# Kernel tuning notes

Measured on AMD Instinct MI355X. Metric: run time of the kernel, lower is better.

Reference implementation:

```python
import jax, jax.numpy as jnp
import numpy as np
import math

EPS = 1e-5
NUM_HEADS = 16


def _ln(x, g, b):
    m = jnp.mean(x, axis=-1, keepdims=True)
    v = jnp.mean(jnp.square(x - m), axis=-1, keepdims=True)
    return (x - m) * jax.lax.rsqrt(v + EPS) * g + b


def setup_inputs() -> dict:
    key = jax.random.key(0)
    ks = jax.random.split(key, 20)
    B, S, D = 16, 256, 1024
    G, L, QL = 576, 64, 16
    V = L * QL
    s = 0.02
    inp = {
        "hidden_states": jax.random.normal(ks[0], (B, S, D), jnp.float32),
        "global_ctx": jax.random.normal(ks[1], (B, G, D), jnp.float32),
        "vision_pos": jax.random.randint(ks[2], (B, G), 0, 1000),
        "instruct_pos": jax.random.randint(ks[3], (B, L), 0, 1000),
        "queries": jax.random.normal(ks[4], (B, V, D), jnp.float32),
        "image_tokens": jax.random.normal(ks[5], (B, V, D), jnp.float32),
        "query_len": QL,
        "W_in": jax.random.normal(ks[6], (D, 2 * D), jnp.float32) * s,
        "W_ctx": jax.random.normal(ks[7], (D, D), jnp.float32) * s,
        "ln_q_g": jnp.ones((D,), jnp.float32),
        "ln_q_b": jnp.zeros((D,), jnp.float32),
        "Wq": jax.random.normal(ks[8], (D, D), jnp.float32) * s,
        "ln_k_g": jnp.ones((D,), jnp.float32),
        "ln_k_b": jnp.zeros((D,), jnp.float32),
        "Wk": jax.random.normal(ks[9], (D, D), jnp.float32) * s,
        "ln_v_g": jnp.ones((D,), jnp.float32),
        "ln_v_b": jnp.zeros((D,), jnp.float32),
        "Wv": jax.random.normal(ks[10], (D, D), jnp.float32) * s,
        "Wo": jax.random.normal(ks[11], (D, D), jnp.float32) * s,
        "norm_g": jnp.ones((D,), jnp.float32),
        "norm_b": jnp.zeros((D,), jnp.float32),
        "W1": jax.random.normal(ks[12], (D, D), jnp.float32) * s,
        "W2": jax.random.normal(ks[13], (D, D), jnp.float32) * s,
    }
    return inp


def reference(hidden_states, global_ctx, vision_pos, instruct_pos, queries,
              image_tokens, query_len, W_in, W_ctx, ln_q_g, ln_q_b, Wq,
              ln_k_g, ln_k_b, Wk, ln_v_g, ln_v_b, Wv, Wo, norm_g, norm_b,
              W1, W2):
    B, V, _ = queries.shape
    D = hidden_states.shape[-1]
    G = global_ctx.shape[1]
    L = instruct_pos.shape[1]
    H = NUM_HEADS
    hd = D // H
    scale = 1.0 / math.sqrt(hd)
    Hq = int(math.sqrt(query_len))          # query grid side
    Hgc = int(math.sqrt(G))                 # ctx grid side
    Hw = Hgc // Hq                          # window side
    Wt = Hw * Hw                            # tokens per window

    residual = image_tokens
    # proj_in on concatenated queries
    pq = jnp.concatenate([queries, image_tokens], axis=-1) @ W_in.T  # (B,V,D)

    # window extraction: (B,Hgc,Wgc,D) -> (B, query_len, Wt, D)
    win = global_ctx.reshape(B, Hq, Hw, Hq, Hw, D)
    win = win.transpose(0, 1, 3, 2, 4, 5).reshape(B, query_len, Wt, D)
    win = win @ W_ctx.T                      # proj_context, shared across L

    # cross-attention: each query v attends only to window (v mod query_len)
    q = _ln(pq, ln_q_g, ln_q_b) @ Wq.T
    q = q.reshape(B, L, query_len, H, hd)
    k = (_ln(win, ln_k_g, ln_k_b) @ Wk.T).reshape(B, query_len, Wt, H, hd)
    v = (_ln(win, ln_v_g, ln_v_b) @ Wv.T).reshape(B, query_len, Wt, H, hd)

    scores = jnp.einsum('blqhd,bqwhd->blqhw', q, k) * scale
    attn = jax.nn.softmax(scores, axis=-1)
    ao = jnp.einsum('blqhw,bqwhd->blqhd', attn, v).reshape(B, V, D)
    ao = ao @ Wo.T

    x = _ln(ao + pq, norm_g, norm_b)
    out = jax.nn.gelu(x @ W1.T, approximate=False) @ W2.T
    return out + residual
```

## Files before the change

### kernel.cpp

```cpp
#include <hip/hip_runtime.h>
#include <cstdint>
#include <cstddef>

typedef unsigned short u16;
typedef __bf16 bf16_t;
typedef bf16_t bf16x8 __attribute__((ext_vector_type(8)));
typedef float f32x4 __attribute__((ext_vector_type(4)));

#define DEV __device__ __forceinline__
#define AS1 __attribute__((address_space(1)))
#define AS3 __attribute__((address_space(3)))

DEV u16 f2bf(float f) {
  unsigned u = __float_as_uint(f);
  u += 0x7fffu + ((u >> 16) & 1u);
  return (u16)(u >> 16);
}
DEV float bf2f(u16 h) {
  return __uint_as_float(((unsigned)h) << 16);
}

struct Cvt9 {
  const float* s[9];
  u16* d[9];
  long cumv[10];
};

__global__ __launch_bounds__(256)
void convert_batch(Cvt9 jobs) {
  const long total = jobs.cumv[9];
  for (long i = (long)blockIdx.x * 256 + threadIdx.x; i < total;
       i += (long)gridDim.x * 256) {
    int j = 0;
#pragma unroll
    for (int t = 0; t < 8; ++t)
      if (i >= jobs.cumv[t + 1]) j = t + 1;
    const long e = (i - jobs.cumv[j]) * 4;
    float4 v = *(const float4*)(jobs.s[j] + e);
    ushort4 o;
    o.x = f2bf(v.x); o.y = f2bf(v.y); o.z = f2bf(v.z); o.w = f2bf(v.w);
    *(ushort4*)(jobs.d[j] + e) = o;
  }
}

__global__ __launch_bounds__(256)
void build_acat(const float* __restrict__ q, const float* __restrict__ it,
                u16* __restrict__ dst) {
  const long total = 16384l * 2048 / 4;
  for (long i = (long)blockIdx.x * 256 + threadIdx.x; i < total;
       i += (long)gridDim.x * 256) {
    long e = i * 4;
    int m = (int)(e >> 11);
    int k = (int)(e & 2047);
    const float* s = (k < 1024) ? (q + (long)m * 1024 + k)
                                : (it + (long)m * 1024 + (k - 1024));
    float4 v = *(const float4*)s;
    ushort4 o;
    o.x = f2bf(v.x); o.y = f2bf(v.y); o.z = f2bf(v.z); o.w = f2bf(v.w);
    *(ushort4*)(dst + e) = o;
  }
}

__global__ __launch_bounds__(256)
void ln_rows(const float* __restrict__ x, const float* __restrict__ g,
             const float* __restrict__ b, u16* __restrict__ out) {
  __shared__ float red[8];
  const int row = blockIdx.x, tid = threadIdx.x;
  const float* xr = x + (size_t)row * 1024;
  float4 v = *(const float4*)(xr + tid * 4);
  float s = v.x + v.y + v.z + v.w;
  float ss = v.x * v.x + v.y * v.y + v.z * v.z + v.w * v.w;
#pragma unroll
  for (int o = 32; o > 0; o >>= 1) { s += __shfl_xor(s, o); ss += __shfl_xor(ss, o); }
  if ((tid & 63) == 0) { red[tid >> 6] = s; red[4 + (tid >> 6)] = ss; }
  __syncthreads();
  s = red[0] + red[1] + red[2] + red[3];
  ss = red[4] + red[5] + red[6] + red[7];
  const float mean = s * 0.0009765625f;
  const float var = ss * 0.0009765625f - mean * mean;
  const float rinv = rsqrtf(var + 1e-5f);
  const int c = tid * 4;
  float4 gg = *(const float4*)(g + c);
  float4 bb = *(const float4*)(b + c);
  ushort4 o4;
  o4.x = f2bf((v.x - mean) * rinv * gg.x + bb.x);
  o4.y = f2bf((v.y - mean) * rinv * gg.y + bb.y);
  o4.z = f2bf((v.z - mean) * rinv * gg.z + bb.z);
  o4.w = f2bf((v.w - mean) * rinv * gg.w + bb.w);
  *(ushort4*)(out + (size_t)row * 1024 + c) = o4;
}

__global__ __launch_bounds__(256)
void ln_kv(const float* __restrict__ winp,
           const float* __restrict__ gk, const float* __restrict__ bk,
           const float* __restrict__ gv, const float* __restrict__ bv,
           u16* __restrict__ kout, u16* __restrict__ vout) {
  __shared__ float red[8];
  const int m = blockIdx.x, tid = threadIdx.x;
  const int b = m / 576, rem = m % 576;
  const int qw = rem / 36, w = rem % 36;
  const int gidx = (qw >> 2) * 144 + (w / 6) * 24 + (qw & 3) * 6 + (w % 6);
  const float* xr = winp + ((size_t)b * 576 + gidx) * 1024;
  float4 v = *(const float4*)(xr + tid * 4);
  float s = v.x + v.y + v.z + v.w;
  float ss = v.x * v.x + v.y * v.y + v.z * v.z + v.w * v.w;
#pragma unroll
  for (int o = 32; o > 0; o >>= 1) { s += __shfl_xor(s, o); ss += __shfl_xor(ss, o); }
  if ((tid & 63) == 0) { red[tid >> 6] = s; red[4 + (tid >> 6)] = ss; }
  __syncthreads();
  s = red[0] + red[1] + red[2] + red[3];
  ss = red[4] + red[5] + red[6] + red[7];
  const float mean = s * 0.0009765625f;
  const float var = ss * 0.0009765625f - mean * mean;
  const float rinv = rsqrtf(var + 1e-5f);
  const int c = tid * 4;
  float4 gg = *(const float4*)(gk + c);
  float4 bb = *(const float4*)(bk + c);
  float4 g2 = *(const float4*)(gv + c);
  float4 b2 = *(const float4*)(bv + c);
  float nx = (v.x - mean) * rinv, ny = (v.y - mean) * rinv;
  float nz = (v.z - mean) * rinv, nw = (v.w - mean) * rinv;
  ushort4 ok, ov;
  ok.x = f2bf(nx * gg.x + bb.x); ok.y = f2bf(ny * gg.y + bb.y);
  ok.z = f2bf(nz * gg.z + bb.z); ok.w = f2bf(nw * gg.w + bb.w);
  ov.x = f2bf(nx * g2.x + b2.x); ov.y = f2bf(ny * g2.y + b2.y);
  ov.z = f2bf(nz * g2.z + b2.z); ov.w = f2bf(nw * g2.w + b2.w);
  *(ushort4*)(kout + (size_t)m * 1024 + c) = ok;
  *(ushort4*)(vout + (size_t)m * 1024 + c) = ov;
}

template <int EPI>
__global__ __launch_bounds__(512, 2)
void gemm256(const u16* __restrict__ A, const u16* __restrict__ Bw,
             u16* __restrict__ outB, float* __restrict__ outF,
             const float* __restrict__ addF, int M, int N, int K) {
  __shared__ __align__(16) u16 lds[2][2][16384];
  const int tid = threadIdx.x;
  const int wave = tid >> 6, lane = tid & 63;
  const int fr = lane & 15, fq = lane >> 4;
  const int swz = (blockIdx.x & 7) * ((int)gridDim.x >> 3) + (blockIdx.x >> 3);
  const int brow = (swz >> 2) << 8;
  const int bcol = (swz & 3) << 8;

  const int srow = tid >> 3;
  const int cgo = ((tid & 7) ^ (srow & 7)) << 3;
  const u16* pa0 = A + (size_t)(brow + srow) * K + cgo;
  const u16* pb0 = Bw + (size_t)(bcol + srow) * K + cgo;
  const size_t rstep = (size_t)64 * K;

  f32x4 acc[8][4];
#pragma unroll
  for (int mf = 0; mf < 8; ++mf)
#pragma unroll
    for (int nf = 0; nf < 4; ++nf) acc[mf][nf] = (f32x4){0.f, 0.f, 0.f, 0.f};

  const int fx = fr & 7;
  const int arow = (wave >> 2) * 128 + fr;
  const int brl = (wave & 3) * 64 + fr;
  const int ck0 = (fq ^ fx) << 3;
  const int ck1 = ((4 + fq) ^ fx) << 3;

  auto STAGE_A = [&](int buf, int kt) {
    const int k0 = kt << 6;
#pragma unroll
    for (int i = 0; i < 4; ++i)
      __builtin_amdgcn_global_load_lds((const AS1 void*)(pa0 + i * rstep + k0),
                                       (AS3 void*)&lds[buf][0][i * 4096 + tid * 8],
                                       16, 0, 0);
  };
  auto STAGE_B = [&](int buf, int kt) {
    const int k0 = kt << 6;
#pragma unroll
    for (int i = 0; i < 4; ++i)
      __builtin_amdgcn_global_load_lds((const AS1 void*)(pb0 + i * rstep + k0),
                                       (AS3 void*)&lds[buf][1][i * 4096 + tid * 8],
                                       16, 0, 0);
  };

  const int NT = K >> 6;
  STAGE_A(0, 0);
  STAGE_B(0, 0);
  __syncthreads();

  bf16x8 a0[4], a1[4], b0[4], b1[4];
  for (int t = 0; t < NT; ++t) {
    const u16* la = &lds[t & 1][0][0];
    const u16* lb = &lds[t & 1][1][0];
    const int nxt = (t + 1) & 1;

#pragma unroll
    for (int nf = 0; nf < 4; ++nf)
      b0[nf] = *(const bf16x8*)&lb[(brl + nf * 16) * 64 + ck0];
#pragma unroll
    for (int mf = 0; mf < 4; ++mf)
      a0[mf] = *(const bf16x8*)&la[(arow + mf * 16) * 64 + ck0];
#pragma unroll
    for (int mf = 0; mf < 4; ++mf)
      a1[mf] = *(const bf16x8*)&la[(arow + 64 + mf * 16) * 64 + ck0];
    if (t + 1 < NT) STAGE_A(nxt, t + 1);
    __builtin_amdgcn_sched_barrier(0);
    __builtin_amdgcn_s_setprio(1);
#pragma unroll
    for (int mf = 0; mf < 4; ++mf)
#pragma unroll
      for (int nf = 0; nf < 4; ++nf)
        acc[mf][nf] = __builtin_amdgcn_mfma_f32_16x16x32_bf16(a0[mf], b0[nf],
                                                              acc[mf][nf], 0, 0, 0);
    __builtin_amdgcn_s_setprio(0);
#pragma unroll
    for (int nf = 0; nf < 4; ++nf)
      b1[nf] = *(const bf16x8*)&lb[(brl + nf * 16) * 64 + ck1];
#pragma unroll
    for (int mf = 0; mf < 4; ++mf)
      a0[mf] = *(const bf16x8*)&la[(arow + mf * 16) * 64 + ck1];
    __builtin_amdgcn_sched_barrier(0);
    __builtin_amdgcn_s_setprio(1);
#pragma unroll
    for (int mf = 0; mf < 4; ++mf)
#pragma unroll
      for (int nf = 0; nf < 4; ++nf)
        acc[4 + mf][nf] = __builtin_amdgcn_mfma_f32_16x16x32_bf16(a1[mf], b0[nf],
                                                                  acc[4 + mf][nf], 0, 0, 0);
    __builtin_amdgcn_s_setprio(0);
#pragma unroll
    for (int mf = 0; mf < 4; ++mf)
      a1[mf] = *(const bf16x8*)&la[(arow + 64 + mf * 16) * 64 + ck1];
    if (t + 1 < NT) STAGE_B(nxt, t + 1);
    __builtin_amdgcn_sched_barrier(0);
    __builtin_amdgcn_s_setprio(1);
#pragma unroll
    for (int mf = 0; mf < 4; ++mf)
#pragma unroll
      for (int nf = 0; nf < 4; ++nf)
        acc[mf][nf] = __builtin_amdgcn_mfma_f32_16x16x32_bf16(a0[mf], b1[nf],
                                                              acc[mf][nf], 0, 0, 0);
    __builtin_amdgcn_s_setprio(0);
    __builtin_amdgcn_sched_barrier(0);
    __builtin_amdgcn_s_setprio(1);
#pragma unroll
    for (int mf = 0; mf < 4; ++mf)
#pragma unroll
      for (int nf = 0; nf < 4; ++nf)
        acc[4 + mf][nf] = __builtin_amdgcn_mfma_f32_16x16x32_bf16(a1[mf], b1[nf],
                                                                  acc[4 + mf][nf], 0, 0, 0);
    __builtin_amdgcn_s_setprio(0);
    __syncthreads();
  }

#pragma unroll
  for (int mf = 0; mf < 8; ++mf) {
    const int row0 = brow + (wave >> 2) * 128 + mf * 16 + fq * 4;
#pragma unroll
    for (int nf = 0; nf < 4; ++nf) {
      const int col = bcol + (wave & 3) * 64 + nf * 16 + fr;
#pragma unroll
      for (int j = 0; j < 4; ++j) {
        const size_t o = (size_t)(row0 + j) * N + col;
        const float vv = acc[mf][nf][j];
        if constexpr (EPI == 0) {
          outB[o] = f2bf(vv);
        } else if constexpr (EPI == 1) {
          outF[o] = vv;
        } else if constexpr (EPI == 2) {
          outF[o] = vv + addF[o];
        } else {
          outB[o] = f2bf(0.5f * vv * (1.0f + erff(vv * 0.70710678118654752f)));
        }
      }
    }
  }
}

__global__ __launch_bounds__(256)
void attn_kernel(const u16* __restrict__ q, const u16* __restrict__ k,
                 const u16* __restrict__ v, u16* __restrict__ ao) {
  __shared__ __align__(16) u16 Qs[64 * 64];
  __shared__ __align__(16) u16 Ks[36 * 64];
  __shared__ __align__(16) u16 Vs[36 * 64];
  __shared__ float Ps[64 * 36];
  const int bid = blockIdx.x;
  const int h = bid & 15, qw = (bid >> 4) & 15, b = bid >> 8;
  const int tid = threadIdx.x;
  const size_t qbase = ((size_t)b * 1024) * 1024 + (size_t)h * 64;
  for (int i = tid; i < 64 * 16; i += 256) {
    int l = i >> 4, d4 = (i & 15) * 4;
    *(ushort4*)&Qs[l * 64 + d4] =
        *(const ushort4*)&q[qbase + (size_t)(l * 16 + qw) * 1024 + d4];
  }
  const size_t kvbase = ((size_t)(b * 16 + qw)) * 36 * 1024 + (size_t)h * 64;
  for (int i = tid; i < 36 * 16; i += 256) {
    int w = i >> 4, d4 = (i & 15) * 4;
    *(ushort4*)&Ks[w * 64 + d4] = *(const ushort4*)&k[kvbase + (size_t)w * 1024 + d4];
    *(ushort4*)&Vs[w * 64 + d4] = *(const ushort4*)&v[kvbase + (size_t)w * 1024 + d4];
  }
  __syncthreads();
  const int l = tid >> 2, quad = tid & 3;
  float sc[9];
#pragma unroll
  for (int wi = 0; wi < 9; ++wi) {
    int w = quad * 9 + wi;
    float acc = 0.f;
#pragma unroll
    for (int dd = 0; dd < 64; dd += 4) {
      ushort4 qv = *(const ushort4*)&Qs[l * 64 + dd];
      ushort4 kv = *(const ushort4*)&Ks[w * 64 + dd];
      acc += bf2f(qv.x) * bf2f(kv.x) + bf2f(qv.y) * bf2f(kv.y) +
             bf2f(qv.z) * bf2f(kv.z) + bf2f(qv.w) * bf2f(kv.w);
    }
    sc[wi] = acc * 0.125f;
  }
  float mx = sc[0];
#pragma unroll
  for (int wi = 1; wi < 9; ++wi) mx = fmaxf(mx, sc[wi]);
  mx = fmaxf(mx, __shfl_xor(mx, 1));
  mx = fmaxf(mx, __shfl_xor(mx, 2));
  float sum = 0.f;
#pragma unroll
  for (int wi = 0; wi < 9; ++wi) { sc[wi] = __expf(sc[wi] - mx); sum += sc[wi]; }
  sum += __shfl_xor(sum, 1);
  sum += __shfl_xor(sum, 2);
  const float inv = 1.0f / sum;
#pragma unroll
  for (int wi = 0; wi < 9; ++wi) Ps[l * 36 + quad * 9 + wi] = sc[wi] * inv;
  __syncthreads();
  float o[16];
#pragma unroll
  for (int dd = 0; dd < 16; ++dd) o[dd] = 0.f;
  for (int w = 0; w < 36; ++w) {
    float p = Ps[l * 36 + w];
#pragma unroll
    for (int dd = 0; dd < 16; dd += 4) {
      ushort4 vv = *(const ushort4*)&Vs[w * 64 + quad * 16 + dd];
      o[dd] += p * bf2f(vv.x); o[dd + 1] += p * bf2f(vv.y);
      o[dd + 2] += p * bf2f(vv.z); o[dd + 3] += p * bf2f(vv.w);
    }
  }
  const size_t obase = qbase + (size_t)(l * 16 + qw) * 1024 + quad * 16;
#pragma unroll
  for (int dd = 0; dd < 16; dd += 4) {
    ushort4 ov;
    ov.x = f2bf(o[dd]); ov.y = f2bf(o[dd + 1]);
    ov.z = f2bf(o[dd + 2]); ov.w = f2bf(o[dd + 3]);
    *(ushort4*)&ao[obase + dd] = ov;
  }
}

extern "C" void kernel_launch(void* const* d_in, const int* in_sizes, int n_in,
                              void* d_out, int out_size, void* d_ws, size_t ws_size,
                              hipStream_t stream) {
  const float* gctx = (const float*)d_in[1];
  const float* queries = (const float*)d_in[4];
  const float* image_tokens = (const float*)d_in[5];
  const float* W_in = (const float*)d_in[7];
  const float* W_ctx = (const float*)d_in[8];
  const float* ln_q_g = (const float*)d_in[9];
  const float* ln_q_b = (const float*)d_in[10];
  const float* Wq = (const float*)d_in[11];
  const float* ln_k_g = (const float*)d_in[12];
  const float* ln_k_b = (const float*)d_in[13];
  const float* Wk = (const float*)d_in[14];
  const float* ln_v_g = (const float*)d_in[15];
  const float* ln_v_b = (const float*)d_in[16];
  const float* Wv = (const float*)d_in[17];
  const float* Wo = (const float*)d_in[18];
  const float* norm_g = (const float*)d_in[19];
  const float* norm_b = (const float*)d_in[20];
  const float* W1 = (const float*)d_in[21];
  const float* W2 = (const float*)d_in[22];
  float* out = (float*)d_out;

  char* ws = (char*)d_ws;
  const size_t MB = 1024 * 1024;
  u16* w_in_b  = (u16*)(ws + 0 * MB);
  u16* w_ctx_b = (u16*)(ws + 4 * MB);
  u16* wq_b    = (u16*)(ws + 6 * MB);
  u16* wk_b    = (u16*)(ws + 8 * MB);
  u16* wv_b    = (u16*)(ws + 10 * MB);
  u16* wo_b    = (u16*)(ws + 12 * MB);
  u16* w1_b    = (u16*)(ws + 14 * MB);
  u16* w2_b    = (u16*)(ws + 16 * MB);
  char* regA = ws + 18 * MB;
  char* regB = regA + 64 * MB;
  char* regC = regB + 36 * MB;

  u16* acat = (u16*)regA;
  u16* pqln = (u16*)regA;
  u16* qmat = (u16*)(regA + 32 * MB);
  u16* vln  = (u16*)regA;
  u16* aoh  = (u16*)regA;
  u16* xmat = (u16*)(regA + 32 * MB);

  float* winp = (float*)regB;
  u16* kmat = (u16*)regB;
  u16* vmat = (u16*)(regB + 18 * MB);
  u16* gout = (u16*)regB;

  u16* gcb = (u16*)regC;
  u16* kln = (u16*)regC;

  float* pq = out;

  Cvt9 jobs;
  const float* srcs[9] = {W_in, W_ctx, Wq, Wk, Wv, Wo, W1, W2, gctx};
  u16* dsts[9] = {w_in_b, w_ctx_b, wq_b, wk_b, wv_b, wo_b, w1_b, w2_b, gcb};
  long sizes[9] = {2048l * 1024, 1048576, 1048576, 1048576, 1048576,
                   1048576, 1048576, 1048576, 9216l * 1024};
  long cum = 0;
  for (int j = 0; j < 9; ++j) {
    jobs.s[j] = srcs[j];
    jobs.d[j] = dsts[j];
    jobs.cumv[j] = cum;
    cum += sizes[j] / 4;
  }
  jobs.cumv[9] = cum;
  convert_batch<<<dim3(2048), dim3(256), 0, stream>>>(jobs);
  build_acat<<<dim3(8192), dim3(256), 0, stream>>>(queries, image_tokens, acat);

  gemm256<1><<<dim3(256), dim3(512), 0, stream>>>(acat, w_in_b, nullptr, pq,
                                                  nullptr, 16384, 1024, 2048);
  ln_rows<<<dim3(16384), dim3(256), 0, stream>>>(pq, ln_q_g, ln_q_b, pqln);
  gemm256<0><<<dim3(256), dim3(512), 0, stream>>>(pqln, wq_b, qmat, nullptr,
                                                  nullptr, 16384, 1024, 1024);
  gemm256<1><<<dim3(144), dim3(512), 0, stream>>>(gcb, w_ctx_b, nullptr, winp,
                                                  nullptr, 9216, 1024, 1024);
  ln_kv<<<dim3(9216), dim3(256), 0, stream>>>(winp, ln_k_g, ln_k_b, ln_v_g,
                                              ln_v_b, kln, vln);
  gemm256<0><<<dim3(144), dim3(512), 0, stream>>>(kln, wk_b, kmat, nullptr,
                                                  nullptr, 9216, 1024, 1024);
  gemm256<0><<<dim3(144), dim3(512), 0, stream>>>(vln, wv_b, vmat, nullptr,
                                                  nullptr, 9216, 1024, 1024);
  attn_kernel<<<dim3(4096), dim3(256), 0, stream>>>(qmat, kmat, vmat, aoh);
  gemm256<2><<<dim3(256), dim3(512), 0, stream>>>(aoh, wo_b, nullptr, pq, pq,
                                                  16384, 1024, 1024);
  ln_rows<<<dim3(16384), dim3(256), 0, stream>>>(pq, norm_g, norm_b, xmat);
  gemm256<3><<<dim3(256), dim3(512), 0, stream>>>(xmat, w1_b, gout, nullptr,
                                                  nullptr, 16384, 1024, 1024);
  gemm256<2><<<dim3(256), dim3(512), 0, stream>>>(gout, w2_b, nullptr, out,
                                                  image_tokens, 16384, 1024, 1024);
}
```

Before: 522.0 us.

## Use MFMA for window attention with transposed V written by GEMM epilogue

Replaces the scalar FP32 dot-product attention with bf16 MFMA 16x16x32 for both QK^T and PV, using padded LDS tiles. Softmax probabilities are stored as bf16 in LDS. The V projection GEMM gets a new epilogue that writes V transposed per window so PV can load contiguous operands. The aim is to cut the scalar ALU and LDS cost of the attention kernel. In exchange it adds zero-padding work, rounds P to bf16, and makes the V GEMM store scattered.

```diff
diff --git a/kernel.cpp b/kernel.cpp
--- a/kernel.cpp
+++ b/kernel.cpp
@@ -263,8 +263,13 @@
           outF[o] = vv;
         } else if constexpr (EPI == 2) {
           outF[o] = vv + addF[o];
+        } else if constexpr (EPI == 3) {
+          outB[o] = f2bf(0.5f * vv * (1.0f + erff(vv * 0.70710678118654752f)));
         } else {
-          outB[o] = f2bf(0.5f * vv * (1.0f + erff(vv * 0.70710678118654752f)));
+          const int gr = row0 + j;
+          const int bqw = gr / 36;
+          const int wl = gr - bqw * 36;
+          outB[(size_t)bqw * 36864 + (size_t)col * 36 + wl] = f2bf(vv);
         }
       }
     }
@@ -273,75 +278,109 @@
 
 __global__ __launch_bounds__(256)
 void attn_kernel(const u16* __restrict__ q, const u16* __restrict__ k,
-                 const u16* __restrict__ v, u16* __restrict__ ao) {
-  __shared__ __align__(16) u16 Qs[64 * 64];
-  __shared__ __align__(16) u16 Ks[36 * 64];
-  __shared__ __align__(16) u16 Vs[36 * 64];
-  __shared__ float Ps[64 * 36];
+                 const u16* __restrict__ vt, u16* __restrict__ ao) {
+  __shared__ __align__(16) u16 Q_lds[64 * 72];
+  __shared__ __align__(16) u16 K_lds[48 * 72];
+  __shared__ __align__(16) u16 Vt_lds[64 * 72];
+  __shared__ __align__(16) u16 P_lds[64 * 72];
   const int bid = blockIdx.x;
   const int h = bid & 15, qw = (bid >> 4) & 15, b = bid >> 8;
   const int tid = threadIdx.x;
-  const size_t qbase = ((size_t)b * 1024) * 1024 + (size_t)h * 64;
+  const int wave = tid >> 6, lane = tid & 63;
+  const int lq = lane & 15, lk = lane >> 4;
+
+  const size_t qbase = (size_t)b * 1048576 + (size_t)h * 64;
   for (int i = tid; i < 64 * 16; i += 256) {
-    int l = i >> 4, d4 = (i & 15) * 4;
-    *(ushort4*)&Qs[l * 64 + d4] =
-        *(const ushort4*)&q[qbase + (size_t)(l * 16 + qw) * 1024 + d4];
-  }
-  const size_t kvbase = ((size_t)(b * 16 + qw)) * 36 * 1024 + (size_t)h * 64;
+    const int l = i >> 4, c4 = (i & 15) * 4;
+    *(ushort4*)&Q_lds[l * 72 + c4] =
+        *(const ushort4*)&q[qbase + (size_t)(l * 16 + qw) * 1024 + c4];
+  }
+  const size_t kvbase = (size_t)((b * 16 + qw) * 36) * 1024 + (size_t)h * 64;
   for (int i = tid; i < 36 * 16; i += 256) {
-    int w = i >> 4, d4 = (i & 15) * 4;
-    *(ushort4*)&Ks[w * 64 + d4] = *(const ushort4*)&k[kvbase + (size_t)w * 1024 + d4];
-    *(ushort4*)&Vs[w * 64 + d4] = *(const ushort4*)&v[kvbase + (size_t)w * 1024 + d4];
+    const int w = i >> 4, c4 = (i & 15) * 4;
+    *(ushort4*)&K_lds[w * 72 + c4] = *(const ushort4*)&k[kvbase + (size_t)w * 1024 + c4];
+  }
+  const size_t vbase = (size_t)(b * 16 + qw) * 36864 + (size_t)h * 2304;
+  for (int i = tid; i < 64 * 9; i += 256) {
+    const int d = i / 9, w4 = (i - d * 9) * 4;
+    *(ushort4*)&Vt_lds[d * 72 + w4] = *(const ushort4*)&vt[vbase + d * 36 + w4];
+  }
+  const ushort4 z4 = {0, 0, 0, 0};
+  for (int i = tid; i < 64 * 7; i += 256) {
+    const int d = i / 7, w = 36 + (i - d * 7) * 4;
+    *(ushort4*)&Vt_lds[d * 72 + w] = z4;
+  }
+  for (int i = tid; i < 64 * 4; i += 256) {
+    const int m = i >> 2, w = 48 + (i & 3) * 4;
+    *(ushort4*)&P_lds[m * 72 + w] = z4;
   }
   __syncthreads();
-  const int l = tid >> 2, quad = tid & 3;
-  float sc[9];
-#pragma unroll
-  for (int wi = 0; wi < 9; ++wi) {
-    int w = quad * 9 + wi;
-    float acc = 0.f;
-#pragma unroll
-    for (int dd = 0; dd < 64; dd += 4) {
-      ushort4 qv = *(const ushort4*)&Qs[l * 64 + dd];
-      ushort4 kv = *(const ushort4*)&Ks[w * 64 + dd];
-      acc += bf2f(qv.x) * bf2f(kv.x) + bf2f(qv.y) * bf2f(kv.y) +
-             bf2f(qv.z) * bf2f(kv.z) + bf2f(qv.w) * bf2f(kv.w);
+
+  bf16x8 qa[2];
+#pragma unroll
+  for (int ks = 0; ks < 2; ++ks)
+    qa[ks] = *(const bf16x8*)&Q_lds[(wave * 16 + lq) * 72 + ks * 32 + lk * 8];
+  f32x4 accs[3];
+#pragma unroll
+  for (int nt = 0; nt < 3; ++nt) accs[nt] = (f32x4){0.f, 0.f, 0.f, 0.f};
+#pragma unroll
+  for (int nt = 0; nt < 3; ++nt)
+#pragma unroll
+    for (int ks = 0; ks < 2; ++ks) {
+      bf16x8 kb = *(const bf16x8*)&K_lds[(nt * 16 + lq) * 72 + ks * 32 + lk * 8];
+      accs[nt] = __builtin_amdgcn_mfma_f32_16x16x32_bf16(qa[ks], kb, accs[nt], 0, 0, 0);
     }
-    sc[wi] = acc * 0.125f;
-  }
-  float mx = sc[0];
-#pragma unroll
-  for (int wi = 1; wi < 9; ++wi) mx = fmaxf(mx, sc[wi]);
-  mx = fmaxf(mx, __shfl_xor(mx, 1));
-  mx = fmaxf(mx, __shfl_xor(mx, 2));
-  float sum = 0.f;
-#pragma unroll
-  for (int wi = 0; wi < 9; ++wi) { sc[wi] = __expf(sc[wi] - mx); sum += sc[wi]; }
-  sum += __shfl_xor(sum, 1);
-  sum += __shfl_xor(sum, 2);
-  const float inv = 1.0f / sum;
-#pragma unroll
-  for (int wi = 0; wi < 9; ++wi) Ps[l * 36 + quad * 9 + wi] = sc[wi] * inv;
+
+  const bool v2ok = (lq < 4);
+#pragma unroll
+  for (int j = 0; j < 4; ++j) {
+    const float s0 = accs[0][j] * 0.125f;
+    const float s1 = accs[1][j] * 0.125f;
+    const float s2 = v2ok ? accs[2][j] * 0.125f : -1e30f;
+    float mx = fmaxf(fmaxf(s0, s1), s2);
+    mx = fmaxf(mx, __shfl_xor(mx, 1));
+    mx = fmaxf(mx, __shfl_xor(mx, 2));
+    mx = fmaxf(mx, __shfl_xor(mx, 4));
+    mx = fmaxf(mx, __shfl_xor(mx, 8));
+    const float e0 = __expf(s0 - mx);
+    const float e1 = __expf(s1 - mx);
+    const float e2 = v2ok ? __expf(s2 - mx) : 0.f;
+    float sm = e0 + e1 + e2;
+    sm += __shfl_xor(sm, 1);
+    sm += __shfl_xor(sm, 2);
+    sm += __shfl_xor(sm, 4);
+    sm += __shfl_xor(sm, 8);
+    const float inv = 1.0f / sm;
+    const int mrow = wave * 16 + lk * 4 + j;
+    P_lds[mrow * 72 + lq] = f2bf(e0 * inv);
+    P_lds[mrow * 72 + 16 + lq] = f2bf(e1 * inv);
+    P_lds[mrow * 72 + 32 + lq] = f2bf(e2 * inv);
+  }
   __syncthreads();
-  float o[16];
-#pragma unroll
-  for (int dd = 0; dd < 16; ++dd) o[dd] = 0.f;
-  for (int w = 0; w < 36; ++w) {
-    float p = Ps[l * 36 + w];
-#pragma unroll
-    for (int dd = 0; dd < 16; dd += 4) {
-      ushort4 vv = *(const ushort4*)&Vs[w * 64 + quad * 16 + dd];
-      o[dd] += p * bf2f(vv.x); o[dd + 1] += p * bf2f(vv.y);
-      o[dd + 2] += p * bf2f(vv.z); o[dd + 3] += p * bf2f(vv.w);
+
+  bf16x8 va[2];
+#pragma unroll
+  for (int ks = 0; ks < 2; ++ks)
+    va[ks] = *(const bf16x8*)&Vt_lds[(wave * 16 + lq) * 72 + ks * 32 + lk * 8];
+  f32x4 acco[4];
+#pragma unroll
+  for (int nt = 0; nt < 4; ++nt) acco[nt] = (f32x4){0.f, 0.f, 0.f, 0.f};
+#pragma unroll
+  for (int nt = 0; nt < 4; ++nt)
+#pragma unroll
+    for (int ks = 0; ks < 2; ++ks) {
+      bf16x8 pb = *(const bf16x8*)&P_lds[(nt * 16 + lq) * 72 + ks * 32 + lk * 8];
+      acco[nt] = __builtin_amdgcn_mfma_f32_16x16x32_bf16(va[ks], pb, acco[nt], 0, 0, 0);
     }
-  }
-  const size_t obase = qbase + (size_t)(l * 16 + qw) * 1024 + quad * 16;
-#pragma unroll
-  for (int dd = 0; dd < 16; dd += 4) {
+
+#pragma unroll
+  for (int nt = 0; nt < 4; ++nt) {
+    const int m = nt * 16 + lq;
+    const int d0 = wave * 16 + lk * 4;
     ushort4 ov;
-    ov.x = f2bf(o[dd]); ov.y = f2bf(o[dd + 1]);
-    ov.z = f2bf(o[dd + 2]); ov.w = f2bf(o[dd + 3]);
-    *(ushort4*)&ao[obase + dd] = ov;
+    ov.x = f2bf(acco[nt][0]); ov.y = f2bf(acco[nt][1]);
+    ov.z = f2bf(acco[nt][2]); ov.w = f2bf(acco[nt][3]);
+    *(ushort4*)&ao[qbase + (size_t)(m * 16 + qw) * 1024 + d0] = ov;
   }
 }
 
@@ -392,7 +431,7 @@
 
   float* winp = (float*)regB;
   u16* kmat = (u16*)regB;
-  u16* vmat = (u16*)(regB + 18 * MB);
+  u16* vtmat = (u16*)(regB + 18 * MB);
   u16* gout = (u16*)regB;
 
   u16* gcb = (u16*)regC;
@@ -427,9 +466,9 @@
                                               ln_v_b, kln, vln);
   gemm256<0><<<dim3(144), dim3(512), 0, stream>>>(kln, wk_b, kmat, nullptr,
                                                   nullptr, 9216, 1024, 1024);
-  gemm256<0><<<dim3(144), dim3(512), 0, stream>>>(vln, wv_b, vmat, nullptr,
+  gemm256<4><<<dim3(144), dim3(512), 0, stream>>>(vln, wv_b, vtmat, nullptr,
                                                   nullptr, 9216, 1024, 1024);
-  attn_kernel<<<dim3(4096), dim3(256), 0, stream>>>(qmat, kmat, vmat, aoh);
+  attn_kernel<<<dim3(4096), dim3(256), 0, stream>>>(qmat, kmat, vtmat, aoh);
   gemm256<2><<<dim3(256), dim3(512), 0, stream>>>(aoh, wo_b, nullptr, pq, pq,
                                                   16384, 1024, 1024);
   ln_rows<<<dim3(16384), dim3(256), 0, stream>>>(pq, norm_g, norm_b, xmat);
```

New measurement: 498.6 us. 4.5% less time.
